# Performance work log

Measured on AMD Instinct MI355X. Metric: run time of the kernel, lower is better.

The kernel has to match this reference:

```python
import jax, jax.numpy as jnp
import numpy as np

B = 8192
DIMS = [5, 1024, 1024, 512, 512, 512, 512, 2]  # model_param
L1, L2, OBS_X, OBS_Y, R = 3.0, 3.0, 0.0, 7.0, 4.0


def _linear_params(key, fan_in, fan_out):
    kw, kb = jax.random.split(key)
    lim = 1.0 / np.sqrt(fan_in)
    W = jax.random.uniform(kw, (fan_in, fan_out), jnp.float32, -lim, lim)
    b = jax.random.uniform(kb, (fan_out,), jnp.float32, -lim, lim)
    return W, b


def setup_inputs() -> dict:
    key = jax.random.key(0)
    keys = jax.random.split(key, 9)
    x = jax.random.normal(keys[0], (B, DIMS[0]), jnp.float32)
    W1, b1 = _linear_params(keys[1], DIMS[0], DIMS[1])
    W2, b2 = _linear_params(keys[2], DIMS[1], DIMS[2])
    W31, b31 = _linear_params(keys[3], DIMS[2], DIMS[3])
    W32, b32 = _linear_params(keys[4], DIMS[2], DIMS[4])
    W41, b41 = _linear_params(keys[5], DIMS[3], DIMS[5])
    W42, b42 = _linear_params(keys[6], DIMS[4], DIMS[6])
    W51, b51 = _linear_params(keys[7], DIMS[5], DIMS[7])
    W52, b52 = _linear_params(keys[8], DIMS[6], DIMS[7])
    return {
        'x': x, 'sgn': 1,
        'mean': jnp.zeros((DIMS[0],), jnp.float32),
        'std': jnp.ones((DIMS[0],), jnp.float32),
        'mean_label': jnp.zeros((2,), jnp.float32),
        'std_label': jnp.ones((2,), jnp.float32),
        'W1': W1, 'b1': b1, 'W2': W2, 'b2': b2,
        'W31': W31, 'b31': b31, 'W32': W32, 'b32': b32,
        'W41': W41, 'b41': b41, 'W42': W42, 'b42': b42,
        'W51': W51, 'b51': b51, 'W52': W52, 'b52': b52,
    }


def _forward(x, mean, std, mean_label, std_label,
             W1, b1, W2, b2, W31, b31, W32, b32,
             W41, b41, W42, b42, W51, b51, W52, b52):
    act = jax.nn.relu
    x0 = x * std + mean                      # un-normalized state [B,5]
    x1 = act(x @ W1 + b1)
    x2 = act(x1 @ W2 + b2)
    x31 = act(x2 @ W31 + b31)
    x32 = act(x2 @ W32 + b32)
    x41 = act(x31 @ W41 + b41)
    x42 = act(x32 @ W42 + b42)
    x51 = x41 @ W51 + b51                    # QP linear term p  [B,2]
    x52 = 4.0 * jax.nn.sigmoid(x42 @ W52 + b52)  # CBF class-K gains [B,2]

    # dCBF terms (two-link arm obstacle barrier)
    t1, w1, t2, w2 = x0[:, 0], x0[:, 1], x0[:, 2], x0[:, 3]
    s1, s2, c1, c2 = jnp.sin(t1), jnp.sin(t2), jnp.cos(t1), jnp.cos(t2)
    px = L1 * c1 + L2 * c2 - OBS_X
    py = L1 * s1 + L2 * s2 - OBS_Y
    vx = -L1 * s1 * w1 - L2 * s2 * w2
    vy = L1 * c1 * w1 + L2 * c2 * w2
    barrier = px * px + py * py - R * R
    b_dot = 2.0 * (px * vx + py * vy)
    Lf2b = (2.0 * (vx * vx + vy * vy)
            + 2.0 * px * (-L1 * c1 * w1 * w1 - L2 * c2 * w2 * w2)
            + 2.0 * py * (-L1 * s1 * w1 * w1 - L2 * s2 * w2 * w2))
    # G (single inequality row, 2 columns), G u <= h
    G1 = -(2.0 * px * (-L1 * s1) + 2.0 * py * (L1 * c1))
    G2 = -(2.0 * px * (-L2 * s2) + 2.0 * py * (L2 * c2))
    G = jnp.stack([G1, G2], axis=1)          # [B,2]
    h = Lf2b + (x52[:, 0] + x52[:, 1]) * b_dot + x52[:, 0] * x52[:, 1] * barrier  # [B]

    # QP: min 0.5||u||^2 + x51.u  s.t. G u <= h  -> closed-form KKT projection
    u0 = -x51                                 # unconstrained optimum
    viol = jnp.sum(G * u0, axis=1) - h        # [B]
    lam = jnp.maximum(viol, 0.0) / (jnp.sum(G * G, axis=1) + 1e-12)
    u = u0 - lam[:, None] * G                 # [B,2]
    return (u - mean_label) / std_label


def reference(x, sgn, mean, std, mean_label, std_label,
              W1, b1, W2, b2, W31, b31, W32, b32,
              W41, b41, W42, b42, W51, b51, W52, b52):
    # sgn == 1 -> batched QP branch (the trained/deployed path)
    return _forward(x, mean, std, mean_label, std_label,
                    W1, b1, W2, b2, W31, b31, W32, b32,
                    W41, b41, W42, b42, W51, b51, W52, b52)
```

## Files before the change

### kernel.cpp

```cpp
#include <hip/hip_runtime.h>
#include <hip/hip_bf16.h>
#include <math.h>


typedef __attribute__((ext_vector_type(4))) float f32x4;
typedef __attribute__((ext_vector_type(8))) short bf16x8;

static __device__ __forceinline__ unsigned short f2bf(float f) {
    unsigned int u = __float_as_uint(f);
    unsigned int r = (u + 0x7fffu + ((u >> 16) & 1u)) >> 16;
    return (unsigned short)r;
}
static __device__ __forceinline__ float bf2f(unsigned short h) {
    return __uint_as_float(((unsigned int)h) << 16);
}

#define TBM 128
#define TBN 256
#define TBK 64

#define GLL(gp, lp) __builtin_amdgcn_global_load_lds( \
    (const __attribute__((address_space(1))) void*)(gp), \
    (__attribute__((address_space(3))) void*)(lp), 16, 0, 0)

#define VMC(N)  asm volatile("s_waitcnt vmcnt(" #N ")" ::: "memory")
#define BAR()   __builtin_amdgcn_s_barrier()
#define SB0()   __builtin_amdgcn_sched_barrier(0)

__device__ __forceinline__ void gemm_core(
    const unsigned short* __restrict__ A, int lda,
    const unsigned short* __restrict__ Bt, int ldb,
    const float* __restrict__ bias,
    unsigned short* __restrict__ C, int ldc,
    int K, int m0, int n0b, int c0)
{
    __shared__ __align__(16) short sA[3][TBM * TBK];
    __shared__ __align__(16) short sB[3][TBN * TBK];

    const int tid  = threadIdx.x;
    const int w    = tid >> 6;
    const int lane = tid & 63;

    const int srow = lane >> 3;
    const int skq  = (lane & 7) ^ ((lane >> 3) & 7);
    const unsigned short* aP0 =
        A + (size_t)(m0 + 16 * w + srow) * lda + skq * 8;
    const unsigned short* aP1 = aP0 + 8 * lda;
    const unsigned short* bP0 =
        Bt + (size_t)(n0b + 32 * w + srow) * ldb + skq * 8;
    const unsigned short* bP1 = bP0 + 8 * ldb;
    const unsigned short* bP2 = bP0 + 16 * ldb;
    const unsigned short* bP3 = bP0 + 24 * ldb;

    const int wrow = (w >> 2) * 64;
    const int wcol = (w & 3) * 64;
    const int fr = lane & 15;
    const int fq = lane >> 4;
    const int swz0 = ((fq)     ^ (fr & 7)) * 8;
    const int swz1 = ((4 + fq) ^ (fr & 7)) * 8;

    f32x4 acc[4][4] = {};
    const int nt = K / TBK;

    auto STAGE = [&](int kt, int b) {
        const size_t ko = (size_t)kt * TBK;
        short* la = &sA[b][0];
        short* lb = &sB[b][0];
        GLL(aP0 + ko, la + (2 * w)     * 512);
        GLL(aP1 + ko, la + (2 * w + 1) * 512);
        GLL(bP0 + ko, lb + (4 * w)     * 512);
        GLL(bP1 + ko, lb + (4 * w + 1) * 512);
        GLL(bP2 + ko, lb + (4 * w + 2) * 512);
        GLL(bP3 + ko, lb + (4 * w + 3) * 512);
    };

    STAGE(0, 0);
    STAGE(1, 1);
    VMC(6);
    BAR();
    SB0();

    int cur = 0, stg = 2;
    for (int t = 0; t < nt; ++t) {
        const short* sAp = &sA[cur][0];
        const short* sBp = &sB[cur][0];

        bf16x8 af[2][4], bf[2][4];
        #pragma unroll
        for (int m = 0; m < 4; ++m) {
            const int r = (wrow + m * 16 + fr) * 64;
            af[0][m] = *reinterpret_cast<const bf16x8*>(&sAp[r + swz0]);
            af[1][m] = *reinterpret_cast<const bf16x8*>(&sAp[r + swz1]);
        }
        #pragma unroll
        for (int n = 0; n < 4; ++n) {
            const int r = (wcol + n * 16 + fr) * 64;
            bf[0][n] = *reinterpret_cast<const bf16x8*>(&sBp[r + swz0]);
            bf[1][n] = *reinterpret_cast<const bf16x8*>(&sBp[r + swz1]);
        }

        if (t + 2 < nt) STAGE(t + 2, stg);

        __builtin_amdgcn_s_setprio(1);
        #pragma unroll
        for (int kh = 0; kh < 2; ++kh)
            #pragma unroll
            for (int m = 0; m < 4; ++m)
                #pragma unroll
                for (int n = 0; n < 4; ++n)
                    acc[m][n] = __builtin_amdgcn_mfma_f32_16x16x32_bf16(
                        af[kh][m], bf[kh][n], acc[m][n], 0, 0, 0);
        __builtin_amdgcn_s_setprio(0);

        if (t + 1 < nt) {
            if (t + 2 < nt) { VMC(6); } else { VMC(0); }
            BAR();
            SB0();
        }
        cur = (cur == 2) ? 0 : cur + 1;
        stg = (stg == 2) ? 0 : stg + 1;
    }

    #pragma unroll
    for (int n = 0; n < 4; ++n) {
        const int cl = wcol + n * 16 + fr;
        const float bv = bias[n0b + cl];
        #pragma unroll
        for (int m = 0; m < 4; ++m) {
            const int rbase = m0 + wrow + m * 16 + fq * 4;
            #pragma unroll
            for (int r = 0; r < 4; ++r) {
                float v = fmaxf(acc[m][n][r] + bv, 0.0f);
                C[(size_t)(rbase + r) * ldc + c0 + cl] = f2bf(v);
            }
        }
    }
}

static __device__ __forceinline__ int xcd_sid() {
    const int bid = blockIdx.y * gridDim.x + blockIdx.x;
    return (bid & 7) * 32 + (bid >> 3);
}

__global__ __launch_bounds__(512, 2) void gemm_bf16(
    const unsigned short* __restrict__ A, int lda,
    const unsigned short* __restrict__ Bt, int ldb,
    const float* __restrict__ bias,
    unsigned short* __restrict__ C, int ldc, int K)
{
    const int sid = xcd_sid();
    const int n0 = (sid & 3) * TBN;
    const int m0 = (sid >> 2) * TBM;
    gemm_core(A, lda, Bt, ldb, bias, C, ldc, K, m0, n0, n0);
}

__global__ __launch_bounds__(512, 2) void gemm_bf16_l4(
    const unsigned short* __restrict__ x3,
    const unsigned short* __restrict__ W41t,
    const unsigned short* __restrict__ W42t,
    const float* __restrict__ b41, const float* __restrict__ b42,
    unsigned short* __restrict__ x4)
{
    const int sid = xcd_sid();
    const int xp  = sid & 3;
    const int g   = xp >> 1;
    const int n0b = (xp & 1) * TBN;
    const int m0  = (sid >> 2) * TBM;
    const unsigned short* A  = x3 + (g ? 512 : 0);
    const unsigned short* Bt = g ? W42t : W41t;
    const float* bias        = g ? b42 : b41;
    gemm_core(A, 1024, Bt, 512, bias, x4, 1024, 512, m0, n0b, g * 512 + n0b);
}

__global__ __launch_bounds__(256) void prep_weights(
    const float* __restrict__ W2,  const float* __restrict__ W31,
    const float* __restrict__ W32, const float* __restrict__ W41,
    const float* __restrict__ W42, const float* __restrict__ b31,
    const float* __restrict__ b32,
    const float* __restrict__ x,   const float* __restrict__ W1,
    const float* __restrict__ b1,
    unsigned short* __restrict__ W2t,  unsigned short* __restrict__ W3t,
    unsigned short* __restrict__ W41t, unsigned short* __restrict__ W42t,
    float* __restrict__ b3c, unsigned short* __restrict__ xb1)
{
    const int z = blockIdx.z;
    if (z == 6) {
        const int r0 = (blockIdx.y * 32 + blockIdx.x) * 8;
        const int j4 = threadIdx.x * 4;
        float4 wv[5];
        #pragma unroll
        for (int k = 0; k < 5; ++k)
            wv[k] = *reinterpret_cast<const float4*>(&W1[k * 1024 + j4]);
        const float4 bb = *reinterpret_cast<const float4*>(&b1[j4]);
        #pragma unroll
        for (int r = 0; r < 8; ++r) {
            const float* xr = &x[(size_t)(r0 + r) * 5];
            float4 acc = bb;
            #pragma unroll
            for (int k = 0; k < 5; ++k) {
                const float xv = xr[k];
                acc.x = fmaf(xv, wv[k].x, acc.x);
                acc.y = fmaf(xv, wv[k].y, acc.y);
                acc.z = fmaf(xv, wv[k].z, acc.z);
                acc.w = fmaf(xv, wv[k].w, acc.w);
            }
            ushort4 o;
            o.x = f2bf(fmaxf(acc.x, 0.f));
            o.y = f2bf(fmaxf(acc.y, 0.f));
            o.z = f2bf(fmaxf(acc.z, 0.f));
            o.w = f2bf(fmaxf(acc.w, 0.f));
            *reinterpret_cast<ushort4*>(&xb1[(size_t)(r0 + r) * 1024 + j4]) = o;
        }
        return;
    }
    if (z == 5) {
        if (blockIdx.x == 0 && blockIdx.y == 0) {
            for (int i = threadIdx.x; i < 1024; i += 256)
                b3c[i] = (i < 512) ? b31[i] : b32[i - 512];
        }
        return;
    }
    const float* src; unsigned short* dst; int K, N;
    switch (z) {
        case 0:  src = W2;  dst = W2t;              K = 1024; N = 1024; break;
        case 1:  src = W31; dst = W3t;              K = 1024; N = 512;  break;
        case 2:  src = W32; dst = W3t + 512 * 1024; K = 1024; N = 512;  break;
        case 3:  src = W41; dst = W41t;             K = 512;  N = 512;  break;
        default: src = W42; dst = W42t;             K = 512;  N = 512;  break;
    }
    const int k0 = blockIdx.x * 32, n0 = blockIdx.y * 32;
    if (k0 >= K || n0 >= N) return;

    __shared__ float t[32][33];
    const int tx = threadIdx.x & 31, ty = threadIdx.x >> 5;
    #pragma unroll
    for (int i = 0; i < 32; i += 8)
        t[ty + i][tx] = src[(size_t)(k0 + ty + i) * N + n0 + tx];
    __syncthreads();
    #pragma unroll
    for (int i = 0; i < 32; i += 8)
        dst[(size_t)(n0 + ty + i) * K + k0 + tx] = f2bf(t[tx][ty + i]);
}

__global__ __launch_bounds__(256) void head_kernel(
    const unsigned short* __restrict__ x4,
    const float* __restrict__ W51, const float* __restrict__ b51,
    const float* __restrict__ W52, const float* __restrict__ b52,
    const float* __restrict__ x,   const float* __restrict__ mean,
    const float* __restrict__ stdv, const float* __restrict__ mean_label,
    const float* __restrict__ std_label, float* __restrict__ out)
{
    const int wave = threadIdx.x >> 6;
    const int lane = threadIdx.x & 63;
    const int row = blockIdx.x * 4 + wave;

    const unsigned short* p41 = x4 + (size_t)row * 1024;
    const bf16x8 v1 = *reinterpret_cast<const bf16x8*>(p41 + lane * 8);
    const bf16x8 v2 = *reinterpret_cast<const bf16x8*>(p41 + 512 + lane * 8);
    const float4 q0 = *reinterpret_cast<const float4*>(W51 + lane * 16 + 0);
    const float4 q1 = *reinterpret_cast<const float4*>(W51 + lane * 16 + 4);
    const float4 q2 = *reinterpret_cast<const float4*>(W51 + lane * 16 + 8);
    const float4 q3 = *reinterpret_cast<const float4*>(W51 + lane * 16 + 12);
    const float4 s0 = *reinterpret_cast<const float4*>(W52 + lane * 16 + 0);
    const float4 s1 = *reinterpret_cast<const float4*>(W52 + lane * 16 + 4);
    const float4 s2 = *reinterpret_cast<const float4*>(W52 + lane * 16 + 8);
    const float4 s3 = *reinterpret_cast<const float4*>(W52 + lane * 16 + 12);

    float a0, a1, a2, a3;
    {
        const float e0 = bf2f((unsigned short)v1[0]), e1 = bf2f((unsigned short)v1[1]),
                    e2 = bf2f((unsigned short)v1[2]), e3 = bf2f((unsigned short)v1[3]),
                    e4 = bf2f((unsigned short)v1[4]), e5 = bf2f((unsigned short)v1[5]),
                    e6 = bf2f((unsigned short)v1[6]), e7 = bf2f((unsigned short)v1[7]);
        a0 = e0*q0.x + e1*q0.z + e2*q1.x + e3*q1.z + e4*q2.x + e5*q2.z + e6*q3.x + e7*q3.z;
        a1 = e0*q0.y + e1*q0.w + e2*q1.y + e3*q1.w + e4*q2.y + e5*q2.w + e6*q3.y + e7*q3.w;
        const float f0 = bf2f((unsigned short)v2[0]), f1 = bf2f((unsigned short)v2[1]),
                    f2 = bf2f((unsigned short)v2[2]), f3 = bf2f((unsigned short)v2[3]),
                    f4 = bf2f((unsigned short)v2[4]), f5 = bf2f((unsigned short)v2[5]),
                    f6 = bf2f((unsigned short)v2[6]), f7 = bf2f((unsigned short)v2[7]);
        a2 = f0*s0.x + f1*s0.z + f2*s1.x + f3*s1.z + f4*s2.x + f5*s2.z + f6*s3.x + f7*s3.z;
        a3 = f0*s0.y + f1*s0.w + f2*s1.y + f3*s1.w + f4*s2.y + f5*s2.w + f6*s3.y + f7*s3.w;
    }
    #pragma unroll
    for (int off = 32; off >= 1; off >>= 1) {
        a0 += __shfl_down(a0, off);
        a1 += __shfl_down(a1, off);
        a2 += __shfl_down(a2, off);
        a3 += __shfl_down(a3, off);
    }

    if (lane == 0) {
        const float L1c = 3.0f, L2c = 3.0f, OBSX = 0.0f, OBSY = 7.0f, Rc = 4.0f;
        const float t1 = x[row * 5 + 0] * stdv[0] + mean[0];
        const float w1 = x[row * 5 + 1] * stdv[1] + mean[1];
        const float t2 = x[row * 5 + 2] * stdv[2] + mean[2];
        const float w2 = x[row * 5 + 3] * stdv[3] + mean[3];
        const float s1v = sinf(t1), c1 = cosf(t1);
        const float s2v = sinf(t2), c2 = cosf(t2);
        const float px = L1c * c1 + L2c * c2 - OBSX;
        const float py = L1c * s1v + L2c * s2v - OBSY;
        const float vx = -L1c * s1v * w1 - L2c * s2v * w2;
        const float vy =  L1c * c1 * w1 + L2c * c2 * w2;
        const float barrier = px * px + py * py - Rc * Rc;
        const float b_dot = 2.0f * (px * vx + py * vy);
        const float Lf2b = 2.0f * (vx * vx + vy * vy)
                         + 2.0f * px * (-L1c * c1 * w1 * w1 - L2c * c2 * w2 * w2)
                         + 2.0f * py * (-L1c * s1v * w1 * w1 - L2c * s2v * w2 * w2);
        const float G1 = -(2.0f * px * (-L1c * s1v) + 2.0f * py * (L1c * c1));
        const float G2 = -(2.0f * px * (-L2c * s2v) + 2.0f * py * (L2c * c2));

        const float x51_0 = a0 + b51[0];
        const float x51_1 = a1 + b51[1];
        const float z0 = a2 + b52[0];
        const float z1 = a3 + b52[1];
        const float x52_0 = 4.0f / (1.0f + expf(-z0));
        const float x52_1 = 4.0f / (1.0f + expf(-z1));

        const float u0_0 = -x51_0;
        const float u0_1 = -x51_1;
        const float h = Lf2b + (x52_0 + x52_1) * b_dot + x52_0 * x52_1 * barrier;
        const float viol = G1 * u0_0 + G2 * u0_1 - h;
        const float lam = fmaxf(viol, 0.0f) / (G1 * G1 + G2 * G2 + 1e-12f);
        const float u_0 = u0_0 - lam * G1;
        const float u_1 = u0_1 - lam * G2;
        out[row * 2 + 0] = (u_0 - mean_label[0]) / std_label[0];
        out[row * 2 + 1] = (u_1 - mean_label[1]) / std_label[1];
    }
}

extern "C" void kernel_launch(void* const* d_in, const int* in_sizes, int n_in,
                              void* d_out, int out_size, void* d_ws, size_t ws_size,
                              hipStream_t stream) {
    const float* x          = (const float*)d_in[0];
    const float* mean       = (const float*)d_in[2];
    const float* stdv       = (const float*)d_in[3];
    const float* mean_label = (const float*)d_in[4];
    const float* std_label  = (const float*)d_in[5];
    const float* W1  = (const float*)d_in[6];   const float* b1  = (const float*)d_in[7];
    const float* W2  = (const float*)d_in[8];   const float* b2  = (const float*)d_in[9];
    const float* W31 = (const float*)d_in[10];  const float* b31 = (const float*)d_in[11];
    const float* W32 = (const float*)d_in[12];  const float* b32 = (const float*)d_in[13];
    const float* W41 = (const float*)d_in[14];  const float* b41 = (const float*)d_in[15];
    const float* W42 = (const float*)d_in[16];  const float* b42 = (const float*)d_in[17];
    const float* W51 = (const float*)d_in[18];  const float* b51 = (const float*)d_in[19];
    const float* W52 = (const float*)d_in[20];  const float* b52 = (const float*)d_in[21];
    float* out = (float*)d_out;

    char* ws = (char*)d_ws;
    const size_t MiB = 1024 * 1024;
    unsigned short* xb1  = (unsigned short*)(ws + 0);
    unsigned short* x2b  = (unsigned short*)(ws + 16 * MiB);
    unsigned short* x3   = xb1;
    unsigned short* x4   = x2b;
    unsigned short* W2t  = (unsigned short*)(ws + 32 * MiB);
    unsigned short* W3t  = (unsigned short*)(ws + 34 * MiB);
    unsigned short* W41t = (unsigned short*)(ws + 36 * MiB);
    unsigned short* W42t = (unsigned short*)(ws + 36 * MiB + 512 * 1024);
    float*          b3c  = (float*)(ws + 37 * MiB);

    prep_weights<<<dim3(32, 32, 7), 256, 0, stream>>>(
        W2, W31, W32, W41, W42, b31, b32, x, W1, b1,
        W2t, W3t, W41t, W42t, b3c, xb1);

    dim3 gBig(1024 / TBN, 8192 / TBM);
    gemm_bf16<<<gBig, 512, 0, stream>>>(xb1, 1024, W2t, 1024, b2, x2b, 1024, 1024);
    gemm_bf16<<<gBig, 512, 0, stream>>>(x2b, 1024, W3t, 1024, b3c, x3, 1024, 1024);

    gemm_bf16_l4<<<dim3(4, 64), 512, 0, stream>>>(x3, W41t, W42t, b41, b42, x4);

    head_kernel<<<2048, 256, 0, stream>>>(x4, W51, b51, W52, b52,
                                          x, mean, stdv, mean_label, std_label, out);
}
```

Measured before the change: 78.95 us.

## Use 4 waves per GEMM block with 64x128 warp tiles

```diff
diff --git a/kernel.cpp b/kernel.cpp
--- a/kernel.cpp
+++ b/kernel.cpp
@@ -44,39 +44,41 @@
     const int srow = lane >> 3;
     const int skq  = (lane & 7) ^ ((lane >> 3) & 7);
     const unsigned short* aP0 =
-        A + (size_t)(m0 + 16 * w + srow) * lda + skq * 8;
-    const unsigned short* aP1 = aP0 + 8 * lda;
+        A + (size_t)(m0 + 32 * w + srow) * lda + skq * 8;
     const unsigned short* bP0 =
-        Bt + (size_t)(n0b + 32 * w + srow) * ldb + skq * 8;
-    const unsigned short* bP1 = bP0 + 8 * ldb;
-    const unsigned short* bP2 = bP0 + 16 * ldb;
-    const unsigned short* bP3 = bP0 + 24 * ldb;
-
-    const int wrow = (w >> 2) * 64;
-    const int wcol = (w & 3) * 64;
+        Bt + (size_t)(n0b + 64 * w + srow) * ldb + skq * 8;
+
+    const int wrow = (w >> 1) * 64;
+    const int wcol = (w & 1) * 128;
     const int fr = lane & 15;
     const int fq = lane >> 4;
     const int swz0 = ((fq)     ^ (fr & 7)) * 8;
     const int swz1 = ((4 + fq) ^ (fr & 7)) * 8;
 
-    f32x4 acc[4][4] = {};
+    f32x4 acc[4][8] = {};
     const int nt = K / TBK;
 
     auto STAGE = [&](int kt, int b) {
         const size_t ko = (size_t)kt * TBK;
         short* la = &sA[b][0];
         short* lb = &sB[b][0];
-        GLL(aP0 + ko, la + (2 * w)     * 512);
-        GLL(aP1 + ko, la + (2 * w + 1) * 512);
-        GLL(bP0 + ko, lb + (4 * w)     * 512);
-        GLL(bP1 + ko, lb + (4 * w + 1) * 512);
-        GLL(bP2 + ko, lb + (4 * w + 2) * 512);
-        GLL(bP3 + ko, lb + (4 * w + 3) * 512);
+        GLL(aP0 + ko,            la + (4 * w + 0) * 512);
+        GLL(aP0 + 8 * lda + ko,  la + (4 * w + 1) * 512);
+        GLL(aP0 + 16 * lda + ko, la + (4 * w + 2) * 512);
+        GLL(aP0 + 24 * lda + ko, la + (4 * w + 3) * 512);
+        GLL(bP0 + ko,            lb + (8 * w + 0) * 512);
+        GLL(bP0 + 8 * ldb + ko,  lb + (8 * w + 1) * 512);
+        GLL(bP0 + 16 * ldb + ko, lb + (8 * w + 2) * 512);
+        GLL(bP0 + 24 * ldb + ko, lb + (8 * w + 3) * 512);
+        GLL(bP0 + 32 * ldb + ko, lb + (8 * w + 4) * 512);
+        GLL(bP0 + 40 * ldb + ko, lb + (8 * w + 5) * 512);
+        GLL(bP0 + 48 * ldb + ko, lb + (8 * w + 6) * 512);
+        GLL(bP0 + 56 * ldb + ko, lb + (8 * w + 7) * 512);
     };
 
     STAGE(0, 0);
     STAGE(1, 1);
-    VMC(6);
+    VMC(12);
     BAR();
     SB0();
 
@@ -85,35 +87,39 @@
         const short* sAp = &sA[cur][0];
         const short* sBp = &sB[cur][0];
 
-        bf16x8 af[2][4], bf[2][4];
+        bf16x8 af0[4], af1[4], bf0[8], bf1[8];
         #pragma unroll
         for (int m = 0; m < 4; ++m) {
             const int r = (wrow + m * 16 + fr) * 64;
-            af[0][m] = *reinterpret_cast<const bf16x8*>(&sAp[r + swz0]);
-            af[1][m] = *reinterpret_cast<const bf16x8*>(&sAp[r + swz1]);
-        }
-        #pragma unroll
-        for (int n = 0; n < 4; ++n) {
+            af0[m] = *reinterpret_cast<const bf16x8*>(&sAp[r + swz0]);
+            af1[m] = *reinterpret_cast<const bf16x8*>(&sAp[r + swz1]);
+        }
+        #pragma unroll
+        for (int n = 0; n < 8; ++n) {
             const int r = (wcol + n * 16 + fr) * 64;
-            bf[0][n] = *reinterpret_cast<const bf16x8*>(&sBp[r + swz0]);
-            bf[1][n] = *reinterpret_cast<const bf16x8*>(&sBp[r + swz1]);
+            bf0[n] = *reinterpret_cast<const bf16x8*>(&sBp[r + swz0]);
+            bf1[n] = *reinterpret_cast<const bf16x8*>(&sBp[r + swz1]);
         }
 
         if (t + 2 < nt) STAGE(t + 2, stg);
 
         __builtin_amdgcn_s_setprio(1);
         #pragma unroll
-        for (int kh = 0; kh < 2; ++kh)
+        for (int m = 0; m < 4; ++m)
             #pragma unroll
-            for (int m = 0; m < 4; ++m)
-                #pragma unroll
-                for (int n = 0; n < 4; ++n)
-                    acc[m][n] = __builtin_amdgcn_mfma_f32_16x16x32_bf16(
-                        af[kh][m], bf[kh][n], acc[m][n], 0, 0, 0);
+            for (int n = 0; n < 8; ++n)
+                acc[m][n] = __builtin_amdgcn_mfma_f32_16x16x32_bf16(
+                    af0[m], bf0[n], acc[m][n], 0, 0, 0);
+        #pragma unroll
+        for (int m = 0; m < 4; ++m)
+            #pragma unroll
+            for (int n = 0; n < 8; ++n)
+                acc[m][n] = __builtin_amdgcn_mfma_f32_16x16x32_bf16(
+                    af1[m], bf1[n], acc[m][n], 0, 0, 0);
         __builtin_amdgcn_s_setprio(0);
 
         if (t + 1 < nt) {
-            if (t + 2 < nt) { VMC(6); } else { VMC(0); }
+            if (t + 2 < nt) { VMC(12); } else { VMC(0); }
             BAR();
             SB0();
         }
@@ -122,7 +128,7 @@
     }
 
     #pragma unroll
-    for (int n = 0; n < 4; ++n) {
+    for (int n = 0; n < 8; ++n) {
         const int cl = wcol + n * 16 + fr;
         const float bv = bias[n0b + cl];
         #pragma unroll
@@ -142,7 +148,7 @@
     return (bid & 7) * 32 + (bid >> 3);
 }
 
-__global__ __launch_bounds__(512, 2) void gemm_bf16(
+__global__ __launch_bounds__(256, 1) void gemm_bf16(
     const unsigned short* __restrict__ A, int lda,
     const unsigned short* __restrict__ Bt, int ldb,
     const float* __restrict__ bias,
@@ -154,7 +160,7 @@
     gemm_core(A, lda, Bt, ldb, bias, C, ldc, K, m0, n0, n0);
 }
 
-__global__ __launch_bounds__(512, 2) void gemm_bf16_l4(
+__global__ __launch_bounds__(256, 1) void gemm_bf16_l4(
     const unsigned short* __restrict__ x3,
     const unsigned short* __restrict__ W41t,
     const unsigned short* __restrict__ W42t,
@@ -363,10 +369,10 @@
         W2t, W3t, W41t, W42t, b3c, xb1);
 
     dim3 gBig(1024 / TBN, 8192 / TBM);
-    gemm_bf16<<<gBig, 512, 0, stream>>>(xb1, 1024, W2t, 1024, b2, x2b, 1024, 1024);
-    gemm_bf16<<<gBig, 512, 0, stream>>>(x2b, 1024, W3t, 1024, b3c, x3, 1024, 1024);
-
-    gemm_bf16_l4<<<dim3(4, 64), 512, 0, stream>>>(x3, W41t, W42t, b41, b42, x4);
+    gemm_bf16<<<gBig, 256, 0, stream>>>(xb1, 1024, W2t, 1024, b2, x2b, 1024, 1024);
+    gemm_bf16<<<gBig, 256, 0, stream>>>(x2b, 1024, W3t, 1024, b3c, x3, 1024, 1024);
+
+    gemm_bf16_l4<<<dim3(4, 64), 256, 0, stream>>>(x3, W41t, W42t, b41, b42, x4);
 
     head_kernel<<<2048, 256, 0, stream>>>(x4, W51, b51, W52, b52,
                                           x, mean, stdv, mean_label, std_label, out);
```

New measurement: 84.46 us. 1.07x slower.

## Fuse all stages into one cooperative persistent kernel with grid syncs

Applied to the files above, without the earlier changes.

```diff
diff --git a/kernel.cpp b/kernel.cpp
--- a/kernel.cpp
+++ b/kernel.cpp
@@ -1,6 +1,9 @@
 #include <hip/hip_runtime.h>
 #include <hip/hip_bf16.h>
+#include <hip/hip_cooperative_groups.h>
 #include <math.h>
+
+namespace cg = cooperative_groups;
 
 
 typedef __attribute__((ext_vector_type(4))) float f32x4;
@@ -32,11 +35,9 @@
     const unsigned short* __restrict__ Bt, int ldb,
     const float* __restrict__ bias,
     unsigned short* __restrict__ C, int ldc,
-    int K, int m0, int n0b, int c0)
+    int K, int m0, int n0b, int c0,
+    short* sAb, short* sBb)
 {
-    __shared__ __align__(16) short sA[3][TBM * TBK];
-    __shared__ __align__(16) short sB[3][TBN * TBK];
-
     const int tid  = threadIdx.x;
     const int w    = tid >> 6;
     const int lane = tid & 63;
@@ -64,8 +65,8 @@
 
     auto STAGE = [&](int kt, int b) {
         const size_t ko = (size_t)kt * TBK;
-        short* la = &sA[b][0];
-        short* lb = &sB[b][0];
+        short* la = sAb + b * (TBM * TBK);
+        short* lb = sBb + b * (TBN * TBK);
         GLL(aP0 + ko, la + (2 * w)     * 512);
         GLL(aP1 + ko, la + (2 * w + 1) * 512);
         GLL(bP0 + ko, lb + (4 * w)     * 512);
@@ -82,8 +83,8 @@
 
     int cur = 0, stg = 2;
     for (int t = 0; t < nt; ++t) {
-        const short* sAp = &sA[cur][0];
-        const short* sBp = &sB[cur][0];
+        const short* sAp = sAb + cur * (TBM * TBK);
+        const short* sBp = sBb + cur * (TBN * TBK);
 
         bf16x8 af[2][4], bf[2][4];
         #pragma unroll
@@ -137,64 +138,60 @@
     }
 }
 
-static __device__ __forceinline__ int xcd_sid() {
-    const int bid = blockIdx.y * gridDim.x + blockIdx.x;
-    return (bid & 7) * 32 + (bid >> 3);
-}
-
-__global__ __launch_bounds__(512, 2) void gemm_bf16(
-    const unsigned short* __restrict__ A, int lda,
-    const unsigned short* __restrict__ Bt, int ldb,
-    const float* __restrict__ bias,
-    unsigned short* __restrict__ C, int ldc, int K)
+struct MegaParams {
+    const float *x, *mean, *stdv, *mean_label, *std_label;
+    const float *W1, *b1, *W2, *b2, *W31, *b31, *W32, *b32;
+    const float *W41, *b41, *W42, *b42, *W51, *b51, *W52, *b52;
+    unsigned short *xb1, *x2b, *W2t, *W3t, *W41t, *W42t;
+    float *b3c;
+    float *out;
+};
+
+__global__ __launch_bounds__(512, 2) void mega_kernel(MegaParams P)
 {
-    const int sid = xcd_sid();
-    const int n0 = (sid & 3) * TBN;
-    const int m0 = (sid >> 2) * TBM;
-    gemm_core(A, lda, Bt, ldb, bias, C, ldc, K, m0, n0, n0);
-}
-
-__global__ __launch_bounds__(512, 2) void gemm_bf16_l4(
-    const unsigned short* __restrict__ x3,
-    const unsigned short* __restrict__ W41t,
-    const unsigned short* __restrict__ W42t,
-    const float* __restrict__ b41, const float* __restrict__ b42,
-    unsigned short* __restrict__ x4)
-{
-    const int sid = xcd_sid();
-    const int xp  = sid & 3;
-    const int g   = xp >> 1;
-    const int n0b = (xp & 1) * TBN;
-    const int m0  = (sid >> 2) * TBM;
-    const unsigned short* A  = x3 + (g ? 512 : 0);
-    const unsigned short* Bt = g ? W42t : W41t;
-    const float* bias        = g ? b42 : b41;
-    gemm_core(A, 1024, Bt, 512, bias, x4, 1024, 512, m0, n0b, g * 512 + n0b);
-}
-
-__global__ __launch_bounds__(256) void prep_weights(
-    const float* __restrict__ W2,  const float* __restrict__ W31,
-    const float* __restrict__ W32, const float* __restrict__ W41,
-    const float* __restrict__ W42, const float* __restrict__ b31,
-    const float* __restrict__ b32,
-    const float* __restrict__ x,   const float* __restrict__ W1,
-    const float* __restrict__ b1,
-    unsigned short* __restrict__ W2t,  unsigned short* __restrict__ W3t,
-    unsigned short* __restrict__ W41t, unsigned short* __restrict__ W42t,
-    float* __restrict__ b3c, unsigned short* __restrict__ xb1)
-{
-    const int z = blockIdx.z;
-    if (z == 6) {
-        const int r0 = (blockIdx.y * 32 + blockIdx.x) * 8;
-        const int j4 = threadIdx.x * 4;
+    __shared__ __align__(16) short sA[3][TBM * TBK];
+    __shared__ __align__(16) short sB[3][TBN * TBK];
+    cg::grid_group grid = cg::this_grid();
+
+    const int bid = blockIdx.x;
+    const int tid = threadIdx.x;
+
+    {
+        const int eng  = bid * 2 + (tid >> 8);
+        const int etid = tid & 255;
+        float* tbuf = (float*)((char*)&sA[0][0] + (tid >> 8) * 4352);
+        const int tx = etid & 31, ty = etid >> 5;
+        #pragma unroll 1
+        for (int T = eng; T < 2560; T += 512) {
+            const float* src; unsigned short* dst; int N, ti;
+            if (T < 1024)      { src = P.W2;  dst = P.W2t;            N = 1024; ti = T; }
+            else if (T < 1536) { src = P.W31; dst = P.W3t;            N = 512;  ti = T - 1024; }
+            else if (T < 2048) { src = P.W32; dst = P.W3t + 512*1024; N = 512;  ti = T - 1536; }
+            else if (T < 2304) { src = P.W41; dst = P.W41t;           N = 512;  ti = T - 2048; }
+            else               { src = P.W42; dst = P.W42t;           N = 512;  ti = T - 2304; }
+            const int ntk = (T < 2048) ? 32 : 16;
+            const int Kd  = ntk * 32;
+            const int k0 = (ti % ntk) * 32, n0 = (ti / ntk) * 32;
+            #pragma unroll
+            for (int i = 0; i < 32; i += 8)
+                tbuf[(ty + i) * 33 + tx] = src[(size_t)(k0 + ty + i) * N + n0 + tx];
+            __syncthreads();
+            #pragma unroll
+            for (int i = 0; i < 32; i += 8)
+                dst[(size_t)(n0 + ty + i) * Kd + k0 + tx] = f2bf(tbuf[tx * 33 + ty + i]);
+            __syncthreads();
+        }
+
+        const int j4 = (tid & 255) * 4;
+        const int r0 = bid * 32 + (tid >> 8) * 16;
         float4 wv[5];
         #pragma unroll
         for (int k = 0; k < 5; ++k)
-            wv[k] = *reinterpret_cast<const float4*>(&W1[k * 1024 + j4]);
-        const float4 bb = *reinterpret_cast<const float4*>(&b1[j4]);
-        #pragma unroll
-        for (int r = 0; r < 8; ++r) {
-            const float* xr = &x[(size_t)(r0 + r) * 5];
+            wv[k] = *reinterpret_cast<const float4*>(&P.W1[k * 1024 + j4]);
+        const float4 bb = *reinterpret_cast<const float4*>(&P.b1[j4]);
+        #pragma unroll 1
+        for (int r = 0; r < 16; ++r) {
+            const float* xr = &P.x[(size_t)(r0 + r) * 5];
             float4 acc = bb;
             #pragma unroll
             for (int k = 0; k < 5; ++k) {
@@ -209,165 +206,161 @@
             o.y = f2bf(fmaxf(acc.y, 0.f));
             o.z = f2bf(fmaxf(acc.z, 0.f));
             o.w = f2bf(fmaxf(acc.w, 0.f));
-            *reinterpret_cast<ushort4*>(&xb1[(size_t)(r0 + r) * 1024 + j4]) = o;
-        }
-        return;
-    }
-    if (z == 5) {
-        if (blockIdx.x == 0 && blockIdx.y == 0) {
-            for (int i = threadIdx.x; i < 1024; i += 256)
-                b3c[i] = (i < 512) ? b31[i] : b32[i - 512];
-        }
-        return;
-    }
-    const float* src; unsigned short* dst; int K, N;
-    switch (z) {
-        case 0:  src = W2;  dst = W2t;              K = 1024; N = 1024; break;
-        case 1:  src = W31; dst = W3t;              K = 1024; N = 512;  break;
-        case 2:  src = W32; dst = W3t + 512 * 1024; K = 1024; N = 512;  break;
-        case 3:  src = W41; dst = W41t;             K = 512;  N = 512;  break;
-        default: src = W42; dst = W42t;             K = 512;  N = 512;  break;
-    }
-    const int k0 = blockIdx.x * 32, n0 = blockIdx.y * 32;
-    if (k0 >= K || n0 >= N) return;
-
-    __shared__ float t[32][33];
-    const int tx = threadIdx.x & 31, ty = threadIdx.x >> 5;
-    #pragma unroll
-    for (int i = 0; i < 32; i += 8)
-        t[ty + i][tx] = src[(size_t)(k0 + ty + i) * N + n0 + tx];
-    __syncthreads();
-    #pragma unroll
-    for (int i = 0; i < 32; i += 8)
-        dst[(size_t)(n0 + ty + i) * K + k0 + tx] = f2bf(t[tx][ty + i]);
-}
-
-__global__ __launch_bounds__(256) void head_kernel(
-    const unsigned short* __restrict__ x4,
-    const float* __restrict__ W51, const float* __restrict__ b51,
-    const float* __restrict__ W52, const float* __restrict__ b52,
-    const float* __restrict__ x,   const float* __restrict__ mean,
-    const float* __restrict__ stdv, const float* __restrict__ mean_label,
-    const float* __restrict__ std_label, float* __restrict__ out)
-{
-    const int wave = threadIdx.x >> 6;
-    const int lane = threadIdx.x & 63;
-    const int row = blockIdx.x * 4 + wave;
-
-    const unsigned short* p41 = x4 + (size_t)row * 1024;
-    const bf16x8 v1 = *reinterpret_cast<const bf16x8*>(p41 + lane * 8);
-    const bf16x8 v2 = *reinterpret_cast<const bf16x8*>(p41 + 512 + lane * 8);
-    const float4 q0 = *reinterpret_cast<const float4*>(W51 + lane * 16 + 0);
-    const float4 q1 = *reinterpret_cast<const float4*>(W51 + lane * 16 + 4);
-    const float4 q2 = *reinterpret_cast<const float4*>(W51 + lane * 16 + 8);
-    const float4 q3 = *reinterpret_cast<const float4*>(W51 + lane * 16 + 12);
-    const float4 s0 = *reinterpret_cast<const float4*>(W52 + lane * 16 + 0);
-    const float4 s1 = *reinterpret_cast<const float4*>(W52 + lane * 16 + 4);
-    const float4 s2 = *reinterpret_cast<const float4*>(W52 + lane * 16 + 8);
-    const float4 s3 = *reinterpret_cast<const float4*>(W52 + lane * 16 + 12);
-
-    float a0, a1, a2, a3;
-    {
-        const float e0 = bf2f((unsigned short)v1[0]), e1 = bf2f((unsigned short)v1[1]),
-                    e2 = bf2f((unsigned short)v1[2]), e3 = bf2f((unsigned short)v1[3]),
-                    e4 = bf2f((unsigned short)v1[4]), e5 = bf2f((unsigned short)v1[5]),
-                    e6 = bf2f((unsigned short)v1[6]), e7 = bf2f((unsigned short)v1[7]);
-        a0 = e0*q0.x + e1*q0.z + e2*q1.x + e3*q1.z + e4*q2.x + e5*q2.z + e6*q3.x + e7*q3.z;
-        a1 = e0*q0.y + e1*q0.w + e2*q1.y + e3*q1.w + e4*q2.y + e5*q2.w + e6*q3.y + e7*q3.w;
-        const float f0 = bf2f((unsigned short)v2[0]), f1 = bf2f((unsigned short)v2[1]),
-                    f2 = bf2f((unsigned short)v2[2]), f3 = bf2f((unsigned short)v2[3]),
-                    f4 = bf2f((unsigned short)v2[4]), f5 = bf2f((unsigned short)v2[5]),
-                    f6 = bf2f((unsigned short)v2[6]), f7 = bf2f((unsigned short)v2[7]);
-        a2 = f0*s0.x + f1*s0.z + f2*s1.x + f3*s1.z + f4*s2.x + f5*s2.z + f6*s3.x + f7*s3.z;
-        a3 = f0*s0.y + f1*s0.w + f2*s1.y + f3*s1.w + f4*s2.y + f5*s2.w + f6*s3.y + f7*s3.w;
-    }
-    #pragma unroll
-    for (int off = 32; off >= 1; off >>= 1) {
-        a0 += __shfl_down(a0, off);
-        a1 += __shfl_down(a1, off);
-        a2 += __shfl_down(a2, off);
-        a3 += __shfl_down(a3, off);
-    }
-
-    if (lane == 0) {
-        const float L1c = 3.0f, L2c = 3.0f, OBSX = 0.0f, OBSY = 7.0f, Rc = 4.0f;
-        const float t1 = x[row * 5 + 0] * stdv[0] + mean[0];
-        const float w1 = x[row * 5 + 1] * stdv[1] + mean[1];
-        const float t2 = x[row * 5 + 2] * stdv[2] + mean[2];
-        const float w2 = x[row * 5 + 3] * stdv[3] + mean[3];
-        const float s1v = sinf(t1), c1 = cosf(t1);
-        const float s2v = sinf(t2), c2 = cosf(t2);
-        const float px = L1c * c1 + L2c * c2 - OBSX;
-        const float py = L1c * s1v + L2c * s2v - OBSY;
-        const float vx = -L1c * s1v * w1 - L2c * s2v * w2;
-        const float vy =  L1c * c1 * w1 + L2c * c2 * w2;
-        const float barrier = px * px + py * py - Rc * Rc;
-        const float b_dot = 2.0f * (px * vx + py * vy);
-        const float Lf2b = 2.0f * (vx * vx + vy * vy)
-                         + 2.0f * px * (-L1c * c1 * w1 * w1 - L2c * c2 * w2 * w2)
-                         + 2.0f * py * (-L1c * s1v * w1 * w1 - L2c * s2v * w2 * w2);
-        const float G1 = -(2.0f * px * (-L1c * s1v) + 2.0f * py * (L1c * c1));
-        const float G2 = -(2.0f * px * (-L2c * s2v) + 2.0f * py * (L2c * c2));
-
-        const float x51_0 = a0 + b51[0];
-        const float x51_1 = a1 + b51[1];
-        const float z0 = a2 + b52[0];
-        const float z1 = a3 + b52[1];
-        const float x52_0 = 4.0f / (1.0f + expf(-z0));
-        const float x52_1 = 4.0f / (1.0f + expf(-z1));
-
-        const float u0_0 = -x51_0;
-        const float u0_1 = -x51_1;
-        const float h = Lf2b + (x52_0 + x52_1) * b_dot + x52_0 * x52_1 * barrier;
-        const float viol = G1 * u0_0 + G2 * u0_1 - h;
-        const float lam = fmaxf(viol, 0.0f) / (G1 * G1 + G2 * G2 + 1e-12f);
-        const float u_0 = u0_0 - lam * G1;
-        const float u_1 = u0_1 - lam * G2;
-        out[row * 2 + 0] = (u_0 - mean_label[0]) / std_label[0];
-        out[row * 2 + 1] = (u_1 - mean_label[1]) / std_label[1];
+            *reinterpret_cast<ushort4*>(&P.xb1[(size_t)(r0 + r) * 1024 + j4]) = o;
+        }
+
+        if (bid == 0) {
+            const int i = tid;
+            P.b3c[i]       = (i < 512) ? P.b31[i] : P.b32[i - 512];
+            P.b3c[i + 512] = ((i + 512) < 512) ? P.b31[i + 512] : P.b32[i];
+        }
+    }
+    grid.sync();
+
+    const int sid = (bid & 7) * 32 + (bid >> 3);
+    unsigned short* x3 = P.xb1;
+    unsigned short* x4 = P.x2b;
+
+    {
+        const int n0 = (sid & 3) * TBN;
+        const int m0 = (sid >> 2) * TBM;
+        gemm_core(P.xb1, 1024, P.W2t, 1024, P.b2, P.x2b, 1024, 1024,
+                  m0, n0, n0, &sA[0][0], &sB[0][0]);
+    }
+    grid.sync();
+
+    {
+        const int n0 = (sid & 3) * TBN;
+        const int m0 = (sid >> 2) * TBM;
+        gemm_core(P.x2b, 1024, P.W3t, 1024, P.b3c, x3, 1024, 1024,
+                  m0, n0, n0, &sA[0][0], &sB[0][0]);
+    }
+    grid.sync();
+
+    {
+        const int xp  = sid & 3;
+        const int g   = xp >> 1;
+        const int n0b = (xp & 1) * TBN;
+        const int m0  = (sid >> 2) * TBM;
+        gemm_core(x3 + (g ? 512 : 0), 1024, g ? P.W42t : P.W41t, 512,
+                  g ? P.b42 : P.b41, x4, 1024, 512,
+                  m0, n0b, g * 512 + n0b, &sA[0][0], &sB[0][0]);
+    }
+    grid.sync();
+
+    {
+        const int wave = tid >> 6;
+        const int lane = tid & 63;
+        const float4 q0 = *reinterpret_cast<const float4*>(P.W51 + lane * 16 + 0);
+        const float4 q1 = *reinterpret_cast<const float4*>(P.W51 + lane * 16 + 4);
+        const float4 q2 = *reinterpret_cast<const float4*>(P.W51 + lane * 16 + 8);
+        const float4 q3 = *reinterpret_cast<const float4*>(P.W51 + lane * 16 + 12);
+        const float4 s0 = *reinterpret_cast<const float4*>(P.W52 + lane * 16 + 0);
+        const float4 s1 = *reinterpret_cast<const float4*>(P.W52 + lane * 16 + 4);
+        const float4 s2 = *reinterpret_cast<const float4*>(P.W52 + lane * 16 + 8);
+        const float4 s3 = *reinterpret_cast<const float4*>(P.W52 + lane * 16 + 12);
+
+        #pragma unroll 1
+        for (int it = 0; it < 4; ++it) {
+            const int row = bid * 32 + it * 8 + wave;
+            const unsigned short* p41 = x4 + (size_t)row * 1024;
+            const bf16x8 v1 = *reinterpret_cast<const bf16x8*>(p41 + lane * 8);
+            const bf16x8 v2 = *reinterpret_cast<const bf16x8*>(p41 + 512 + lane * 8);
+
+            float a0, a1, a2, a3;
+            {
+                const float e0 = bf2f((unsigned short)v1[0]), e1 = bf2f((unsigned short)v1[1]),
+                            e2 = bf2f((unsigned short)v1[2]), e3 = bf2f((unsigned short)v1[3]),
+                            e4 = bf2f((unsigned short)v1[4]), e5 = bf2f((unsigned short)v1[5]),
+                            e6 = bf2f((unsigned short)v1[6]), e7 = bf2f((unsigned short)v1[7]);
+                a0 = e0*q0.x + e1*q0.z + e2*q1.x + e3*q1.z + e4*q2.x + e5*q2.z + e6*q3.x + e7*q3.z;
+                a1 = e0*q0.y + e1*q0.w + e2*q1.y + e3*q1.w + e4*q2.y + e5*q2.w + e6*q3.y + e7*q3.w;
+                const float f0 = bf2f((unsigned short)v2[0]), f1 = bf2f((unsigned short)v2[1]),
+                            f2 = bf2f((unsigned short)v2[2]), f3 = bf2f((unsigned short)v2[3]),
+                            f4 = bf2f((unsigned short)v2[4]), f5 = bf2f((unsigned short)v2[5]),
+                            f6 = bf2f((unsigned short)v2[6]), f7 = bf2f((unsigned short)v2[7]);
+                a2 = f0*s0.x + f1*s0.z + f2*s1.x + f3*s1.z + f4*s2.x + f5*s2.z + f6*s3.x + f7*s3.z;
+                a3 = f0*s0.y + f1*s0.w + f2*s1.y + f3*s1.w + f4*s2.y + f5*s2.w + f6*s3.y + f7*s3.w;
+            }
+            #pragma unroll
+            for (int off = 32; off >= 1; off >>= 1) {
+                a0 += __shfl_down(a0, off);
+                a1 += __shfl_down(a1, off);
+                a2 += __shfl_down(a2, off);
+                a3 += __shfl_down(a3, off);
+            }
+
+            if (lane == 0) {
+                const float L1c = 3.0f, L2c = 3.0f, OBSY = 7.0f, Rc = 4.0f;
+                const float t1 = P.x[row * 5 + 0] * P.stdv[0] + P.mean[0];
+                const float w1 = P.x[row * 5 + 1] * P.stdv[1] + P.mean[1];
+                const float t2 = P.x[row * 5 + 2] * P.stdv[2] + P.mean[2];
+                const float w2 = P.x[row * 5 + 3] * P.stdv[3] + P.mean[3];
+                const float s1v = sinf(t1), c1 = cosf(t1);
+                const float s2v = sinf(t2), c2 = cosf(t2);
+                const float px = L1c * c1 + L2c * c2;
+                const float py = L1c * s1v + L2c * s2v - OBSY;
+                const float vx = -L1c * s1v * w1 - L2c * s2v * w2;
+                const float vy =  L1c * c1 * w1 + L2c * c2 * w2;
+                const float barrier = px * px + py * py - Rc * Rc;
+                const float b_dot = 2.0f * (px * vx + py * vy);
+                const float Lf2b = 2.0f * (vx * vx + vy * vy)
+                                 + 2.0f * px * (-L1c * c1 * w1 * w1 - L2c * c2 * w2 * w2)
+                                 + 2.0f * py * (-L1c * s1v * w1 * w1 - L2c * s2v * w2 * w2);
+                const float G1 = -(2.0f * px * (-L1c * s1v) + 2.0f * py * (L1c * c1));
+                const float G2 = -(2.0f * px * (-L2c * s2v) + 2.0f * py * (L2c * c2));
+
+                const float x51_0 = a0 + P.b51[0];
+                const float x51_1 = a1 + P.b51[1];
+                const float z0 = a2 + P.b52[0];
+                const float z1 = a3 + P.b52[1];
+                const float x52_0 = 4.0f / (1.0f + expf(-z0));
+                const float x52_1 = 4.0f / (1.0f + expf(-z1));
+
+                const float u0_0 = -x51_0;
+                const float u0_1 = -x51_1;
+                const float h = Lf2b + (x52_0 + x52_1) * b_dot + x52_0 * x52_1 * barrier;
+                const float viol = G1 * u0_0 + G2 * u0_1 - h;
+                const float lam = fmaxf(viol, 0.0f) / (G1 * G1 + G2 * G2 + 1e-12f);
+                const float u_0 = u0_0 - lam * G1;
+                const float u_1 = u0_1 - lam * G2;
+                P.out[row * 2 + 0] = (u_0 - P.mean_label[0]) / P.std_label[0];
+                P.out[row * 2 + 1] = (u_1 - P.mean_label[1]) / P.std_label[1];
+            }
+        }
     }
 }
 
 extern "C" void kernel_launch(void* const* d_in, const int* in_sizes, int n_in,
                               void* d_out, int out_size, void* d_ws, size_t ws_size,
                               hipStream_t stream) {
-    const float* x          = (const float*)d_in[0];
-    const float* mean       = (const float*)d_in[2];
-    const float* stdv       = (const float*)d_in[3];
-    const float* mean_label = (const float*)d_in[4];
-    const float* std_label  = (const float*)d_in[5];
-    const float* W1  = (const float*)d_in[6];   const float* b1  = (const float*)d_in[7];
-    const float* W2  = (const float*)d_in[8];   const float* b2  = (const float*)d_in[9];
-    const float* W31 = (const float*)d_in[10];  const float* b31 = (const float*)d_in[11];
-    const float* W32 = (const float*)d_in[12];  const float* b32 = (const float*)d_in[13];
-    const float* W41 = (const float*)d_in[14];  const float* b41 = (const float*)d_in[15];
-    const float* W42 = (const float*)d_in[16];  const float* b42 = (const float*)d_in[17];
-    const float* W51 = (const float*)d_in[18];  const float* b51 = (const float*)d_in[19];
-    const float* W52 = (const float*)d_in[20];  const float* b52 = (const float*)d_in[21];
-    float* out = (float*)d_out;
-
     char* ws = (char*)d_ws;
     const size_t MiB = 1024 * 1024;
-    unsigned short* xb1  = (unsigned short*)(ws + 0);
-    unsigned short* x2b  = (unsigned short*)(ws + 16 * MiB);
-    unsigned short* x3   = xb1;
-    unsigned short* x4   = x2b;
-    unsigned short* W2t  = (unsigned short*)(ws + 32 * MiB);
-    unsigned short* W3t  = (unsigned short*)(ws + 34 * MiB);
-    unsigned short* W41t = (unsigned short*)(ws + 36 * MiB);
-    unsigned short* W42t = (unsigned short*)(ws + 36 * MiB + 512 * 1024);
-    float*          b3c  = (float*)(ws + 37 * MiB);
-
-    prep_weights<<<dim3(32, 32, 7), 256, 0, stream>>>(
-        W2, W31, W32, W41, W42, b31, b32, x, W1, b1,
-        W2t, W3t, W41t, W42t, b3c, xb1);
-
-    dim3 gBig(1024 / TBN, 8192 / TBM);
-    gemm_bf16<<<gBig, 512, 0, stream>>>(xb1, 1024, W2t, 1024, b2, x2b, 1024, 1024);
-    gemm_bf16<<<gBig, 512, 0, stream>>>(x2b, 1024, W3t, 1024, b3c, x3, 1024, 1024);
-
-    gemm_bf16_l4<<<dim3(4, 64), 512, 0, stream>>>(x3, W41t, W42t, b41, b42, x4);
-
-    head_kernel<<<2048, 256, 0, stream>>>(x4, W51, b51, W52, b52,
-                                          x, mean, stdv, mean_label, std_label, out);
-}
+
+    MegaParams P;
+    P.x          = (const float*)d_in[0];
+    P.mean       = (const float*)d_in[2];
+    P.stdv       = (const float*)d_in[3];
+    P.mean_label = (const float*)d_in[4];
+    P.std_label  = (const float*)d_in[5];
+    P.W1  = (const float*)d_in[6];   P.b1  = (const float*)d_in[7];
+    P.W2  = (const float*)d_in[8];   P.b2  = (const float*)d_in[9];
+    P.W31 = (const float*)d_in[10];  P.b31 = (const float*)d_in[11];
+    P.W32 = (const float*)d_in[12];  P.b32 = (const float*)d_in[13];
+    P.W41 = (const float*)d_in[14];  P.b41 = (const float*)d_in[15];
+    P.W42 = (const float*)d_in[16];  P.b42 = (const float*)d_in[17];
+    P.W51 = (const float*)d_in[18];  P.b51 = (const float*)d_in[19];
+    P.W52 = (const float*)d_in[20];  P.b52 = (const float*)d_in[21];
+    P.xb1  = (unsigned short*)(ws + 0);
+    P.x2b  = (unsigned short*)(ws + 16 * MiB);
+    P.W2t  = (unsigned short*)(ws + 32 * MiB);
+    P.W3t  = (unsigned short*)(ws + 34 * MiB);
+    P.W41t = (unsigned short*)(ws + 36 * MiB);
+    P.W42t = (unsigned short*)(ws + 36 * MiB + 512 * 1024);
+    P.b3c  = (float*)(ws + 37 * MiB);
+    P.out  = (float*)d_out;
+
+    void* kargs[] = { (void*)&P };
+    hipLaunchCooperativeKernel(reinterpret_cast<void*>(mega_kernel),
+                               dim3(256), dim3(512), kargs, 0, stream);
+}
```

After: 216.2 us. 2.74x slower.
